# Optimization experiments

Hardware: AMD Instinct MI355X
Metric: run time of the kernel (lower is better)

## Reference

```python
import jax, jax.numpy as jnp
import numpy as np

N, M, C, IN, OUT = 65536, 512, 512, 256, 256
EPS = 1e-8


def setup_inputs() -> dict:
    key = jax.random.key(0)
    ks = jax.random.split(key, 12)
    d = {}
    d["x"] = jax.random.normal(ks[0], (1, IN), jnp.float32)
    d["memory"] = jax.random.normal(ks[1], (1, N, M), jnp.float32) * 0.05
    d["prev_read"] = jax.random.normal(ks[2], (1, M), jnp.float32) * 0.05
    d["h"] = jnp.ones((1, C), jnp.float32)
    d["c"] = jnp.ones((1, C), jnp.float32)
    d["read_state"] = jnp.zeros((1, N), jnp.float32)
    d["write_state"] = jnp.zeros((1, N), jnp.float32)
    d["W_ih"] = jax.random.normal(ks[3], (4 * C, IN + M), jnp.float32) * 0.02
    d["b_ih"] = jax.random.normal(ks[4], (4 * C,), jnp.float32) * 0.01
    d["W_hh"] = jax.random.normal(ks[5], (4 * C, C), jnp.float32) * 0.02
    d["b_hh"] = jax.random.normal(ks[6], (4 * C,), jnp.float32) * 0.01
    d["W_read"] = jax.random.normal(ks[7], (M + 6, C), jnp.float32) * 0.02
    d["b_read"] = jnp.zeros((M + 6,), jnp.float32)
    d["W_write"] = jax.random.normal(ks[8], (3 * M + 6, C), jnp.float32) * 0.02
    d["b_write"] = jnp.zeros((3 * M + 6,), jnp.float32)
    d["W_out"] = jax.random.normal(ks[9], (OUT, C + M), jnp.float32) * 0.02
    d["b_out"] = jnp.zeros((OUT,), jnp.float32)
    return d


def _address(head_out, w_prev, memory):
    # head_out: [B, M+6(+...)]; returns sharpened addressing weights [B, N]
    key_v = head_out[:, :M]
    beta = jax.nn.softplus(head_out[:, M:M + 1])          # [B,1]
    g = jax.nn.sigmoid(head_out[:, M + 1:M + 2])          # [B,1]
    shift = jax.nn.softmax(head_out[:, M + 2:M + 5], axis=1)  # [B,3]
    gamma = 1.0 + jax.nn.softplus(head_out[:, M + 5:M + 6])   # [B,1]
    # content addressing: cosine similarity over memory rows
    a = memory + EPS                                      # [B,N,M]
    b = key_v[:, None, :] + EPS                           # [B,1,M]
    dot = jnp.sum(a * b, axis=-1)                         # [B,N]
    na = jnp.maximum(jnp.sqrt(jnp.sum(a * a, axis=-1)), EPS)
    nb = jnp.maximum(jnp.sqrt(jnp.sum(b * b, axis=-1)), EPS)
    cos = dot / (na * nb)
    w_context = jax.nn.softmax(beta * cos, axis=1)        # [B,N]
    # NOTE: original code swaps args -> g gates the PREVIOUS weights
    w_interp = g * w_prev + (1.0 - g) * w_context
    # circular shift via 3-tap correlation (conv1d with circular pad)
    w_pad = jnp.concatenate([w_interp[:, -1:], w_interp, w_interp[:, :1]], axis=1)
    w_shift = (w_pad[:, :-2] * shift[:, 0:1]
               + w_pad[:, 1:-1] * shift[:, 1:2]
               + w_pad[:, 2:] * shift[:, 2:3])
    power = w_shift ** gamma
    return power / (jnp.sum(power, axis=1, keepdims=True) + EPS)


def reference(x, memory, prev_read, h, c, read_state, write_state,
              W_ih, b_ih, W_hh, b_hh, W_read, b_read, W_write, b_write,
              W_out, b_out):
    # LSTMCell controller (torch gate order: i, f, g, o)
    inp = jnp.concatenate([x, prev_read], axis=1)                   # [B, IN+M]
    gates = inp @ W_ih.T + b_ih + h @ W_hh.T + b_hh                 # [B, 4C]
    i_g, f_g, g_g, o_g = jnp.split(gates, 4, axis=1)
    c_new = jax.nn.sigmoid(f_g) * c + jax.nn.sigmoid(i_g) * jnp.tanh(g_g)
    h_new = jax.nn.sigmoid(o_g) * jnp.tanh(c_new)

    # read head
    r_out = h_new @ W_read.T + b_read
    w_r = _address(r_out, read_state, memory)                       # [B,N]
    # faithful to torch.matmul([B,N],[B,N,M]).sum(1): sums weights over batch
    read = jnp.einsum('n,bnm->bm', jnp.sum(w_r, axis=0), memory)    # [B,M]

    # write head
    w_out_head = h_new @ W_write.T + b_write
    w_w = _address(w_out_head, write_state, memory)                 # [B,N]
    erase = jax.nn.sigmoid(w_out_head[:, M + 6:2 * M + 6])          # [B,M]
    add = w_out_head[:, 2 * M + 6:3 * M + 6]                        # [B,M]
    memory_new = memory * (1.0 - w_w[:, :, None] * erase[:, None, :]) \
                 + w_w[:, :, None] * add[:, None, :]                # [B,N,M]

    out = jax.nn.sigmoid(jnp.concatenate([h_new, read], axis=1) @ W_out.T + b_out)
    del memory_new  # state update; torch forward returns only the output
    return out
```

## Files before the change

### kernel.cpp

```cpp
#include <hip/hip_runtime.h>
#include <math.h>

#define EPS 1e-8f
#define NN 65536
#define MAGIC 1.0f

#define WS_GATES 0
#define WS_HNEW  2048
#define WS_ROUT  2560
#define WS_PMAX  3104
#define WS_PEXP  5152
#define WS_S     7200
#define WS_PART  72992
#define WS_FLAGG 204064
#define WS_FLAGP 204192
#define WS_PART2 204448
#define WS_FLAG2 220832
#define WS_BF    262144
#define WS_PARTB 17039360
#define WS_PSUMB 18087936

typedef float f32x2 __attribute__((ext_vector_type(2)));

__device__ __forceinline__ float wave_sum(float v) {
    for (int o = 32; o > 0; o >>= 1) v += __shfl_xor(v, o);
    return v;
}
__device__ __forceinline__ float sigm(float x) { return 1.f / (1.f + expf(-x)); }
__device__ __forceinline__ float softplusf_(float x) {
    return x > 20.f ? x : log1pf(expf(x));
}
__device__ __forceinline__ float dot4(float4 a, float4 b) {
    return a.x * b.x + a.y * b.y + a.z * b.z + a.w * b.w;
}
__device__ __forceinline__ float4 ld4(const float* p) { return *(const float4*)p; }

__device__ __forceinline__ float ald(const float* p) {
    return __hip_atomic_load(p, __ATOMIC_RELAXED, __HIP_MEMORY_SCOPE_AGENT);
}
__device__ __forceinline__ float ald_acq(const float* p) {
    return __hip_atomic_load(p, __ATOMIC_ACQUIRE, __HIP_MEMORY_SCOPE_AGENT);
}
__device__ __forceinline__ void ast(float* p, float v) {
    __hip_atomic_store(p, v, __ATOMIC_RELAXED, __HIP_MEMORY_SCOPE_AGENT);
}
__device__ __forceinline__ void ast_rel(float* p, float v) {
    __hip_atomic_store(p, v, __ATOMIC_RELEASE, __HIP_MEMORY_SCOPE_AGENT);
}

__device__ __forceinline__ unsigned pk8(float4 v) {
    int u = __builtin_amdgcn_cvt_pk_fp8_f32(v.x, v.y, 0, false);
    u = __builtin_amdgcn_cvt_pk_fp8_f32(v.z, v.w, u, true);
    return (unsigned)u;
}

__global__ __launch_bounds__(256) void k_front(const float* __restrict__ x,
                                               const float* __restrict__ pr,
                                               const float* __restrict__ h,
                                               const float* __restrict__ c,
                                               const float* __restrict__ W_ih,
                                               const float* __restrict__ b_ih,
                                               const float* __restrict__ W_hh,
                                               const float* __restrict__ b_hh,
                                               const float* __restrict__ W_read,
                                               const float* __restrict__ b_read,
                                               float* __restrict__ ws) {
    const int b = blockIdx.x, t = threadIdx.x;
    const int lane = t & 63, wv = t >> 6;
    __shared__ float sh[512];

    if (b < 128) {
        #pragma unroll
        for (int i = 0; i < 4; ++i) {
            const int row = b * 16 + wv * 4 + i;
            const float* wi = W_ih + (size_t)row * 768;
            const float* wh = W_hh + (size_t)row * 512;
            float acc = dot4(ld4(wi + lane * 4), ld4(x + lane * 4))
                      + dot4(ld4(wi + 256 + lane * 4), ld4(pr + lane * 4))
                      + dot4(ld4(wi + 512 + lane * 4), ld4(pr + 256 + lane * 4))
                      + dot4(ld4(wh + lane * 4), ld4(h + lane * 4))
                      + dot4(ld4(wh + 256 + lane * 4), ld4(h + 256 + lane * 4));
            acc = wave_sum(acc);
            if (lane == 0) ast(ws + WS_GATES + row, acc + b_ih[row] + b_hh[row]);
        }
        __syncthreads();
        if (t == 0) ast_rel(ws + WS_FLAGG + b, MAGIC);
    }

    if (wv == 0) {
        int cap = 0;
        for (;;) {
            float v0 = ald_acq(ws + WS_FLAGG + lane);
            float v1 = ald_acq(ws + WS_FLAGG + 64 + lane);
            if (__all(v0 == MAGIC && v1 == MAGIC)) break;
            __builtin_amdgcn_s_sleep(1);
            if (++cap > (1 << 20)) break;
        }
    }
    __syncthreads();

    for (int j = t; j < 512; j += 256) {
        float ig = ald(ws + WS_GATES + j);
        float fg = ald(ws + WS_GATES + 512 + j);
        float gg = ald(ws + WS_GATES + 1024 + j);
        float og = ald(ws + WS_GATES + 1536 + j);
        float cn = sigm(fg) * c[j] + sigm(ig) * tanhf(gg);
        float hn = sigm(og) * tanhf(cn);
        sh[j] = hn;
        if (b == 0) ws[WS_HNEW + j] = hn;
    }
    __syncthreads();
    const int o = b * 4 + wv;
    if (o < 518) {
        const float* wr = W_read + (size_t)o * 512;
        float acc = dot4(ld4(wr + lane * 4), ld4(sh + lane * 4))
                  + dot4(ld4(wr + 256 + lane * 4), ld4(sh + 256 + lane * 4));
        acc = wave_sum(acc);
        if (lane == 0) ws[WS_ROUT + o] = acc + b_read[o];
    }
}

__global__ __launch_bounds__(256) void k_cos(const float* __restrict__ mem,
                                             float* __restrict__ ws) {
    const int t = threadIdx.x, lane = t & 63, wv = t >> 6;
    const int gw = blockIdx.x * 4 + wv;
    const float* key = ws + WS_ROUT;
    unsigned char* wsb = (unsigned char*)(ws + WS_BF);
    float4 ka = ld4(key + lane * 4);
    float4 kb = ld4(key + 256 + lane * 4);
    ka.x += EPS; ka.y += EPS; ka.z += EPS; ka.w += EPS;
    kb.x += EPS; kb.y += EPS; kb.z += EPS; kb.w += EPS;
    const float nb = fmaxf(__builtin_amdgcn_sqrtf(
                        wave_sum(dot4(ka, ka) + dot4(kb, kb))), EPS);
    const float beta = softplusf_(key[512]);
    float* sp = ws + WS_S;

    float4 va[4], vb[4], xa[4], xb[4];
    #pragma unroll
    for (int i = 0; i < 4; ++i) {
        const size_t n = (size_t)gw + i * 8192;
        va[i] = ld4(mem + n * 512 + lane * 4);
        vb[i] = ld4(mem + n * 512 + 256 + lane * 4);
    }
    #pragma unroll
    for (int i = 0; i < 4; ++i) {
        const size_t n = (size_t)gw + (4 + i) * 8192;
        xa[i] = ld4(mem + n * 512 + lane * 4);
        xb[i] = ld4(mem + n * 512 + 256 + lane * 4);
    }

    float m = -1e30f, e = 0.f;
    #pragma unroll
    for (int grp = 0; grp < 2; ++grp) {
        float d[4], q[4];
        #pragma unroll
        for (int i = 0; i < 4; ++i) {
            const size_t n = (size_t)gw + (grp * 4 + i) * 8192;
            *(unsigned*)(wsb + n * 512 + lane * 4) = pk8(va[i]);
            *(unsigned*)(wsb + n * 512 + 256 + lane * 4) = pk8(vb[i]);
            float4 wa = va[i], wb = vb[i];
            wa.x += EPS; wa.y += EPS; wa.z += EPS; wa.w += EPS;
            wb.x += EPS; wb.y += EPS; wb.z += EPS; wb.w += EPS;
            d[i] = dot4(wa, ka) + dot4(wb, kb);
            q[i] = dot4(wa, wa) + dot4(wb, wb);
        }
        if (grp == 0) {
            #pragma unroll
            for (int i = 0; i < 4; ++i) { va[i] = xa[i]; vb[i] = xb[i]; }
        }
        #pragma unroll
        for (int o = 32; o > 0; o >>= 1) {
            #pragma unroll
            for (int i = 0; i < 4; ++i) {
                d[i] += __shfl_xor(d[i], o);
                q[i] += __shfl_xor(q[i], o);
            }
        }
        float sv[4];
        #pragma unroll
        for (int i = 0; i < 4; ++i) {
            float na = fmaxf(__builtin_amdgcn_sqrtf(q[i]), EPS);
            sv[i] = beta * d[i] * __builtin_amdgcn_rcpf(na * nb);
        }
        float mysv = sv[0];
        if (lane == 1) mysv = sv[1];
        if (lane == 2) mysv = sv[2];
        if (lane == 3) mysv = sv[3];
        if (lane < 4) sp[gw + (grp * 4 + lane) * 8192] = mysv;
        float gm = fmaxf(fmaxf(sv[0], sv[1]), fmaxf(sv[2], sv[3]));
        float nm = fmaxf(m, gm);
        e = e * __expf(m - nm) + __expf(sv[0] - nm) + __expf(sv[1] - nm)
          + __expf(sv[2] - nm) + __expf(sv[3] - nm);
        m = nm;
    }

    __shared__ float sm[4], se[4];
    if (lane == 0) { sm[wv] = m; se[wv] = e; }
    __syncthreads();
    if (t == 0) {
        float M = fmaxf(fmaxf(sm[0], sm[1]), fmaxf(sm[2], sm[3]));
        float E = se[0] * __expf(sm[0] - M) + se[1] * __expf(sm[1] - M) +
                  se[2] * __expf(sm[2] - M) + se[3] * __expf(sm[3] - M);
        ws[WS_PMAX + blockIdx.x] = M;
        ws[WS_PEXP + blockIdx.x] = E;
    }
}

__global__ __launch_bounds__(256) void k_read(const float* __restrict__ rs,
                                              float* __restrict__ ws) {
    const int bb = blockIdx.x, t = threadIdx.x;
    const int lane = t & 63, wv = t >> 6;
    __shared__ float s_m[4], s_e[4];
    __shared__ float wi_l[34];
    __shared__ float pl[32];
    __shared__ float sacc[3][512];

    float m = -1e30f, e = 0.f;
    #pragma unroll
    for (int i = 0; i < 8; ++i) {
        float bm = ws[WS_PMAX + t + 256 * i], be = ws[WS_PEXP + t + 256 * i];
        float nm = fmaxf(m, bm);
        e = e * __expf(m - nm) + be * __expf(bm - nm);
        m = nm;
    }
    for (int o = 32; o > 0; o >>= 1) {
        float om = __shfl_xor(m, o), oe = __shfl_xor(e, o);
        float nm = fmaxf(m, om);
        e = e * __expf(m - nm) + oe * __expf(om - nm);
        m = nm;
    }
    if (lane == 0) { s_m[wv] = m; s_e[wv] = e; }
    __syncthreads();
    const float mx = fmaxf(fmaxf(s_m[0], s_m[1]), fmaxf(s_m[2], s_m[3]));
    const float Z = s_e[0] * __expf(s_m[0] - mx) + s_e[1] * __expf(s_m[1] - mx)
                  + s_e[2] * __expf(s_m[2] - mx) + s_e[3] * __expf(s_m[3] - mx);
    const float invZ = 1.f / Z;
    const float g = sigm(ws[WS_ROUT + 513]);
    float a3 = ws[WS_ROUT + 514], b3 = ws[WS_ROUT + 515], c3 = ws[WS_ROUT + 516];
    float mm = fmaxf(a3, fmaxf(b3, c3));
    float ea = __expf(a3 - mm), eb = __expf(b3 - mm), ec = __expf(c3 - mm);
    float ss = ea + eb + ec;
    const float s0 = ea / ss, s1 = eb / ss, s2 = ec / ss;
    const float gamma = 1.f + softplusf_(ws[WS_ROUT + 517]);

    const int start = bb * 32;
    if (t < 34) {
        int idx = (start - 1 + t) & (NN - 1);
        wi_l[t] = g * rs[idx] + (1.f - g) * __expf(ws[WS_S + idx] - mx) * invZ;
    }
    __syncthreads();
    float ps = 0.f;
    if (t < 32) {
        float wsh = wi_l[t] * s0 + wi_l[t + 1] * s1 + wi_l[t + 2] * s2;
        float pv = __powf(wsh, gamma);
        pl[t] = pv;
        ps = pv;
    }
    ps = wave_sum(ps);
    if (t == 0) ws[WS_PSUMB + bb] = ps;
    __syncthreads();

    const unsigned char* slab =
        (const unsigned char*)(ws + WS_BF) + (size_t)(start + wv * 8) * 512;
    float a0 = 0.f, a1 = 0.f, a2 = 0.f, a3f = 0.f,
          a4 = 0.f, a5 = 0.f, a6 = 0.f, a7 = 0.f;
    #pragma unroll
    for (int r = 0; r < 8; ++r) {
        float w = pl[wv * 8 + r];
        uint2 q = *(const uint2*)(slab + (size_t)r * 512 + lane * 8);
        f32x2 f0 = __builtin_amdgcn_cvt_pk_f32_fp8(q.x, false);
        f32x2 f1 = __builtin_amdgcn_cvt_pk_f32_fp8(q.x, true);
        f32x2 f2 = __builtin_amdgcn_cvt_pk_f32_fp8(q.y, false);
        f32x2 f3 = __builtin_amdgcn_cvt_pk_f32_fp8(q.y, true);
        a0 += w * f0.x;  a1 += w * f0.y;
        a2 += w * f1.x;  a3f += w * f1.y;
        a4 += w * f2.x;  a5 += w * f2.y;
        a6 += w * f3.x;  a7 += w * f3.y;
    }
    if (wv) {
        float* sw = sacc[wv - 1];
        sw[0 * 64 + lane] = a0; sw[1 * 64 + lane] = a1;
        sw[2 * 64 + lane] = a2; sw[3 * 64 + lane] = a3f;
        sw[4 * 64 + lane] = a4; sw[5 * 64 + lane] = a5;
        sw[6 * 64 + lane] = a6; sw[7 * 64 + lane] = a7;
    }
    __syncthreads();
    if (!wv) {
        #pragma unroll
        for (int i = 0; i < 3; ++i) {
            const float* sw = sacc[i];
            a0 += sw[0 * 64 + lane]; a1 += sw[1 * 64 + lane];
            a2 += sw[2 * 64 + lane]; a3f += sw[3 * 64 + lane];
            a4 += sw[4 * 64 + lane]; a5 += sw[5 * 64 + lane];
            a6 += sw[6 * 64 + lane]; a7 += sw[7 * 64 + lane];
        }
        float* pp = ws + WS_PARTB + (size_t)bb * 512 + lane * 8;
        *(float4*)pp = make_float4(a0, a1, a2, a3f);
        *(float4*)(pp + 4) = make_float4(a4, a5, a6, a7);
    }
}

__global__ __launch_bounds__(512) void k_out(const float* __restrict__ W_out,
                                             const float* __restrict__ b_out,
                                             float* __restrict__ ws,
                                             float* __restrict__ out) {
    const int b = blockIdx.x, t = threadIdx.x;
    const int lane = t & 63, wv = t >> 6;
    __shared__ float rd[512];
    __shared__ float s_z[8];

    {
        float s = 0.f;
        #pragma unroll
        for (int r = 0; r < 8; ++r)
            s += ws[WS_PARTB + (size_t)(8 * b + r) * 512 + t];
        ws[WS_PART + (size_t)b * 512 + t] = s;
    }
    __syncthreads();
    if (t == 0) ast_rel(ws + WS_FLAGP + b, MAGIC);
    if (b >= 32) return;

    if (wv == 0) {
        int cap = 0;
        for (;;) {
            float v0 = ald_acq(ws + WS_FLAGP + lane);
            float v1 = ald_acq(ws + WS_FLAGP + 64 + lane);
            float v2 = ald_acq(ws + WS_FLAGP + 128 + lane);
            float v3 = ald_acq(ws + WS_FLAGP + 192 + lane);
            if (__all(v0 == MAGIC && v1 == MAGIC && v2 == MAGIC && v3 == MAGIC))
                break;
            __builtin_amdgcn_s_sleep(1);
            if (++cap > (1 << 20)) break;
        }
    }
    __syncthreads();
    {
        float s = 0.f;
        #pragma unroll
        for (int r = 0; r < 8; ++r)
            s += ws[WS_PART + (size_t)(8 * b + r) * 512 + t];
        ws[WS_PART2 + (size_t)b * 512 + t] = s;
    }
    __syncthreads();
    if (t == 0) ast_rel(ws + WS_FLAG2 + b, MAGIC);
    if (wv == 0) {
        int cap = 0;
        for (;;) {
            float v = ald_acq(ws + WS_FLAG2 + (lane & 31));
            if (__all(v == MAGIC)) break;
            __builtin_amdgcn_s_sleep(1);
            if (++cap > (1 << 20)) break;
        }
    }
    __syncthreads();
    float z = 0.f;
    #pragma unroll
    for (int i = 0; i < 4; ++i) z += ws[WS_PSUMB + t + 512 * i];
    z = wave_sum(z);
    if (lane == 0) s_z[wv] = z;
    __syncthreads();
    float Zp = 0.f;
    for (int i = 0; i < 8; ++i) Zp += s_z[i];
    const float invZp = 1.f / (Zp + EPS);
    {
        float s = 0.f;
        #pragma unroll
        for (int r = 0; r < 32; ++r)
            s += ws[WS_PART2 + (size_t)r * 512 + t];
        rd[t] = s * invZp;
    }
    __syncthreads();
    const int o = b * 8 + wv;
    const float* wo = W_out + (size_t)o * 1024;
    float a = dot4(ld4(wo + lane * 4), ld4(ws + WS_HNEW + lane * 4))
            + dot4(ld4(wo + 256 + lane * 4), ld4(ws + WS_HNEW + 256 + lane * 4))
            + dot4(ld4(wo + 512 + lane * 4), ld4(rd + lane * 4))
            + dot4(ld4(wo + 768 + lane * 4), ld4(rd + 256 + lane * 4));
    a = wave_sum(a);
    if (lane == 0) out[o] = sigm(a + b_out[o]);
}

extern "C" void kernel_launch(void* const* d_in, const int* in_sizes, int n_in,
                              void* d_out, int out_size, void* d_ws, size_t ws_size,
                              hipStream_t stream) {
    const float* x          = (const float*)d_in[0];
    const float* memory     = (const float*)d_in[1];
    const float* prev_read  = (const float*)d_in[2];
    const float* h          = (const float*)d_in[3];
    const float* c          = (const float*)d_in[4];
    const float* read_state = (const float*)d_in[5];
    const float* W_ih   = (const float*)d_in[7];
    const float* b_ih   = (const float*)d_in[8];
    const float* W_hh   = (const float*)d_in[9];
    const float* b_hh   = (const float*)d_in[10];
    const float* W_read = (const float*)d_in[11];
    const float* b_read = (const float*)d_in[12];
    const float* W_out  = (const float*)d_in[15];
    const float* b_out  = (const float*)d_in[16];
    float* ws  = (float*)d_ws;
    float* out = (float*)d_out;

    k_front<<<130, 256, 0, stream>>>(x, prev_read, h, c, W_ih, b_ih, W_hh, b_hh,
                                     W_read, b_read, ws);
    k_cos<<<2048, 256, 0, stream>>>(memory, ws);
    k_read<<<2048, 256, 0, stream>>>(read_state, ws);
    k_out<<<256, 512, 0, stream>>>(W_out, b_out, ws, out);
}
```

Measured before the change: 66.48 us.

## Fuse four kernels into two using flag-based inter-block synchronization

Merges the LSTM/read-projection front kernel into the cosine-similarity kernel, and the read-accumulation kernel into the output kernel. Workgroups spin on global release/acquire flags in place of kernel boundaries. This removes two launch gaps and their tail drain. In exchange, 2048 blocks now all wait on flags set by the first 130 (and later the first 2048). That relies on enough blocks being co-resident or scheduled in order, and costs polling traffic plus idle waiting blocks.

```diff
diff --git a/kernel.cpp b/kernel.cpp
--- a/kernel.cpp
+++ b/kernel.cpp
@@ -16,9 +16,11 @@
 #define WS_FLAGP 204192
 #define WS_PART2 204448
 #define WS_FLAG2 220832
+#define WS_FLAGR 220864
 #define WS_BF    262144
 #define WS_PARTB 17039360
 #define WS_PSUMB 18087936
+#define WS_FLAGB 18089984
 
 typedef float f32x2 __attribute__((ext_vector_type(2)));
 
@@ -54,17 +56,18 @@
     return (unsigned)u;
 }
 
-__global__ __launch_bounds__(256) void k_front(const float* __restrict__ x,
-                                               const float* __restrict__ pr,
-                                               const float* __restrict__ h,
-                                               const float* __restrict__ c,
-                                               const float* __restrict__ W_ih,
-                                               const float* __restrict__ b_ih,
-                                               const float* __restrict__ W_hh,
-                                               const float* __restrict__ b_hh,
-                                               const float* __restrict__ W_read,
-                                               const float* __restrict__ b_read,
-                                               float* __restrict__ ws) {
+__global__ __launch_bounds__(256) void k_fc(const float* __restrict__ x,
+                                            const float* __restrict__ pr,
+                                            const float* __restrict__ h,
+                                            const float* __restrict__ c,
+                                            const float* __restrict__ W_ih,
+                                            const float* __restrict__ b_ih,
+                                            const float* __restrict__ W_hh,
+                                            const float* __restrict__ b_hh,
+                                            const float* __restrict__ W_read,
+                                            const float* __restrict__ b_read,
+                                            const float* __restrict__ mem,
+                                            float* __restrict__ ws) {
     const int b = blockIdx.x, t = threadIdx.x;
     const int lane = t & 63, wv = t >> 6;
     __shared__ float sh[512];
@@ -87,43 +90,55 @@
         if (t == 0) ast_rel(ws + WS_FLAGG + b, MAGIC);
     }
 
+    if (b < 130) {
+        if (wv == 0) {
+            int cap = 0;
+            for (;;) {
+                float v0 = ald_acq(ws + WS_FLAGG + lane);
+                float v1 = ald_acq(ws + WS_FLAGG + 64 + lane);
+                if (__all(v0 == MAGIC && v1 == MAGIC)) break;
+                __builtin_amdgcn_s_sleep(1);
+                if (++cap > (1 << 20)) break;
+            }
+        }
+        __syncthreads();
+        for (int j = t; j < 512; j += 256) {
+            float ig = ald(ws + WS_GATES + j);
+            float fg = ald(ws + WS_GATES + 512 + j);
+            float gg = ald(ws + WS_GATES + 1024 + j);
+            float og = ald(ws + WS_GATES + 1536 + j);
+            float cn = sigm(fg) * c[j] + sigm(ig) * tanhf(gg);
+            float hn = sigm(og) * tanhf(cn);
+            sh[j] = hn;
+            if (b == 0) ws[WS_HNEW + j] = hn;
+        }
+        __syncthreads();
+        const int o = b * 4 + wv;
+        if (o < 518) {
+            const float* wr = W_read + (size_t)o * 512;
+            float acc = dot4(ld4(wr + lane * 4), ld4(sh + lane * 4))
+                      + dot4(ld4(wr + 256 + lane * 4), ld4(sh + 256 + lane * 4));
+            acc = wave_sum(acc);
+            if (lane == 0) ws[WS_ROUT + o] = acc + b_read[o];
+        }
+        __syncthreads();
+        if (t == 0) ast_rel(ws + WS_FLAGR + b, MAGIC);
+    }
+
     if (wv == 0) {
         int cap = 0;
         for (;;) {
-            float v0 = ald_acq(ws + WS_FLAGG + lane);
-            float v1 = ald_acq(ws + WS_FLAGG + 64 + lane);
-            if (__all(v0 == MAGIC && v1 == MAGIC)) break;
+            float v0 = ald_acq(ws + WS_FLAGR + lane);
+            float v1 = ald_acq(ws + WS_FLAGR + 64 + lane);
+            float v2 = ald_acq(ws + WS_FLAGR + 128 + (lane & 1));
+            if (__all(v0 == MAGIC && v1 == MAGIC && v2 == MAGIC)) break;
             __builtin_amdgcn_s_sleep(1);
             if (++cap > (1 << 20)) break;
         }
     }
     __syncthreads();
 
-    for (int j = t; j < 512; j += 256) {
-        float ig = ald(ws + WS_GATES + j);
-        float fg = ald(ws + WS_GATES + 512 + j);
-        float gg = ald(ws + WS_GATES + 1024 + j);
-        float og = ald(ws + WS_GATES + 1536 + j);
-        float cn = sigm(fg) * c[j] + sigm(ig) * tanhf(gg);
-        float hn = sigm(og) * tanhf(cn);
-        sh[j] = hn;
-        if (b == 0) ws[WS_HNEW + j] = hn;
-    }
-    __syncthreads();
-    const int o = b * 4 + wv;
-    if (o < 518) {
-        const float* wr = W_read + (size_t)o * 512;
-        float acc = dot4(ld4(wr + lane * 4), ld4(sh + lane * 4))
-                  + dot4(ld4(wr + 256 + lane * 4), ld4(sh + 256 + lane * 4));
-        acc = wave_sum(acc);
-        if (lane == 0) ws[WS_ROUT + o] = acc + b_read[o];
-    }
-}
-
-__global__ __launch_bounds__(256) void k_cos(const float* __restrict__ mem,
-                                             float* __restrict__ ws) {
-    const int t = threadIdx.x, lane = t & 63, wv = t >> 6;
-    const int gw = blockIdx.x * 4 + wv;
+    const int gw = b * 4 + wv;
     const float* key = ws + WS_ROUT;
     unsigned char* wsb = (unsigned char*)(ws + WS_BF);
     float4 ka = ld4(key + lane * 4);
@@ -201,19 +216,24 @@
         float M = fmaxf(fmaxf(sm[0], sm[1]), fmaxf(sm[2], sm[3]));
         float E = se[0] * __expf(sm[0] - M) + se[1] * __expf(sm[1] - M) +
                   se[2] * __expf(sm[2] - M) + se[3] * __expf(sm[3] - M);
-        ws[WS_PMAX + blockIdx.x] = M;
-        ws[WS_PEXP + blockIdx.x] = E;
-    }
-}
-
-__global__ __launch_bounds__(256) void k_read(const float* __restrict__ rs,
-                                              float* __restrict__ ws) {
+        ws[WS_PMAX + b] = M;
+        ws[WS_PEXP + b] = E;
+    }
+}
+
+__global__ __launch_bounds__(256) void k_ro(const float* __restrict__ rs,
+                                            const float* __restrict__ W_out,
+                                            const float* __restrict__ b_out,
+                                            float* __restrict__ ws,
+                                            float* __restrict__ out) {
     const int bb = blockIdx.x, t = threadIdx.x;
     const int lane = t & 63, wv = t >> 6;
     __shared__ float s_m[4], s_e[4];
     __shared__ float wi_l[34];
     __shared__ float pl[32];
     __shared__ float sacc[3][512];
+    __shared__ float rd[512];
+    __shared__ float s_z[4];
 
     float m = -1e30f, e = 0.f;
     #pragma unroll
@@ -260,66 +280,76 @@
     if (t == 0) ws[WS_PSUMB + bb] = ps;
     __syncthreads();
 
-    const unsigned char* slab =
-        (const unsigned char*)(ws + WS_BF) + (size_t)(start + wv * 8) * 512;
-    float a0 = 0.f, a1 = 0.f, a2 = 0.f, a3f = 0.f,
-          a4 = 0.f, a5 = 0.f, a6 = 0.f, a7 = 0.f;
-    #pragma unroll
-    for (int r = 0; r < 8; ++r) {
-        float w = pl[wv * 8 + r];
-        uint2 q = *(const uint2*)(slab + (size_t)r * 512 + lane * 8);
-        f32x2 f0 = __builtin_amdgcn_cvt_pk_f32_fp8(q.x, false);
-        f32x2 f1 = __builtin_amdgcn_cvt_pk_f32_fp8(q.x, true);
-        f32x2 f2 = __builtin_amdgcn_cvt_pk_f32_fp8(q.y, false);
-        f32x2 f3 = __builtin_amdgcn_cvt_pk_f32_fp8(q.y, true);
-        a0 += w * f0.x;  a1 += w * f0.y;
-        a2 += w * f1.x;  a3f += w * f1.y;
-        a4 += w * f2.x;  a5 += w * f2.y;
-        a6 += w * f3.x;  a7 += w * f3.y;
-    }
-    if (wv) {
-        float* sw = sacc[wv - 1];
-        sw[0 * 64 + lane] = a0; sw[1 * 64 + lane] = a1;
-        sw[2 * 64 + lane] = a2; sw[3 * 64 + lane] = a3f;
-        sw[4 * 64 + lane] = a4; sw[5 * 64 + lane] = a5;
-        sw[6 * 64 + lane] = a6; sw[7 * 64 + lane] = a7;
-    }
-    __syncthreads();
-    if (!wv) {
-        #pragma unroll
-        for (int i = 0; i < 3; ++i) {
-            const float* sw = sacc[i];
-            a0 += sw[0 * 64 + lane]; a1 += sw[1 * 64 + lane];
-            a2 += sw[2 * 64 + lane]; a3f += sw[3 * 64 + lane];
-            a4 += sw[4 * 64 + lane]; a5 += sw[5 * 64 + lane];
-            a6 += sw[6 * 64 + lane]; a7 += sw[7 * 64 + lane];
-        }
-        float* pp = ws + WS_PARTB + (size_t)bb * 512 + lane * 8;
-        *(float4*)pp = make_float4(a0, a1, a2, a3f);
-        *(float4*)(pp + 4) = make_float4(a4, a5, a6, a7);
-    }
-}
-
-__global__ __launch_bounds__(512) void k_out(const float* __restrict__ W_out,
-                                             const float* __restrict__ b_out,
-                                             float* __restrict__ ws,
-                                             float* __restrict__ out) {
-    const int b = blockIdx.x, t = threadIdx.x;
-    const int lane = t & 63, wv = t >> 6;
-    __shared__ float rd[512];
-    __shared__ float s_z[8];
-
     {
+        const unsigned char* slab =
+            (const unsigned char*)(ws + WS_BF) + (size_t)(start + wv * 8) * 512;
+        float a0 = 0.f, a1 = 0.f, a2 = 0.f, a3f = 0.f,
+              a4 = 0.f, a5 = 0.f, a6 = 0.f, a7 = 0.f;
+        #pragma unroll
+        for (int r = 0; r < 8; ++r) {
+            float w = pl[wv * 8 + r];
+            uint2 q = *(const uint2*)(slab + (size_t)r * 512 + lane * 8);
+            f32x2 f0 = __builtin_amdgcn_cvt_pk_f32_fp8(q.x, false);
+            f32x2 f1 = __builtin_amdgcn_cvt_pk_f32_fp8(q.x, true);
+            f32x2 f2 = __builtin_amdgcn_cvt_pk_f32_fp8(q.y, false);
+            f32x2 f3 = __builtin_amdgcn_cvt_pk_f32_fp8(q.y, true);
+            a0 += w * f0.x;  a1 += w * f0.y;
+            a2 += w * f1.x;  a3f += w * f1.y;
+            a4 += w * f2.x;  a5 += w * f2.y;
+            a6 += w * f3.x;  a7 += w * f3.y;
+        }
+        if (wv) {
+            float* sw = sacc[wv - 1];
+            sw[0 * 64 + lane] = a0; sw[1 * 64 + lane] = a1;
+            sw[2 * 64 + lane] = a2; sw[3 * 64 + lane] = a3f;
+            sw[4 * 64 + lane] = a4; sw[5 * 64 + lane] = a5;
+            sw[6 * 64 + lane] = a6; sw[7 * 64 + lane] = a7;
+        }
+        __syncthreads();
+        if (!wv) {
+            #pragma unroll
+            for (int i = 0; i < 3; ++i) {
+                const float* sw = sacc[i];
+                a0 += sw[0 * 64 + lane]; a1 += sw[1 * 64 + lane];
+                a2 += sw[2 * 64 + lane]; a3f += sw[3 * 64 + lane];
+                a4 += sw[4 * 64 + lane]; a5 += sw[5 * 64 + lane];
+                a6 += sw[6 * 64 + lane]; a7 += sw[7 * 64 + lane];
+            }
+            float* pp = ws + WS_PARTB + (size_t)bb * 512 + lane * 8;
+            *(float4*)pp = make_float4(a0, a1, a2, a3f);
+            *(float4*)(pp + 4) = make_float4(a4, a5, a6, a7);
+        }
+    }
+    __syncthreads();
+    if (t == 0) ast_rel(ws + WS_FLAGB + bb, MAGIC);
+
+    if (bb >= 256) return;
+    if (wv == 0) {
+        int cap = 0;
+        for (;;) {
+            bool ok = true;
+            #pragma unroll
+            for (int k = 0; k < 32; ++k)
+                ok &= (ald_acq(ws + WS_FLAGB + k * 64 + lane) == MAGIC);
+            if (__all(ok)) break;
+            __builtin_amdgcn_s_sleep(1);
+            if (++cap > (1 << 20)) break;
+        }
+    }
+    __syncthreads();
+    #pragma unroll
+    for (int cc = 0; cc < 2; ++cc) {
+        const int col = t + cc * 256;
         float s = 0.f;
         #pragma unroll
         for (int r = 0; r < 8; ++r)
-            s += ws[WS_PARTB + (size_t)(8 * b + r) * 512 + t];
-        ws[WS_PART + (size_t)b * 512 + t] = s;
-    }
-    __syncthreads();
-    if (t == 0) ast_rel(ws + WS_FLAGP + b, MAGIC);
-    if (b >= 32) return;
-
+            s += ws[WS_PARTB + (size_t)(8 * bb + r) * 512 + col];
+        ws[WS_PART + (size_t)bb * 512 + col] = s;
+    }
+    __syncthreads();
+    if (t == 0) ast_rel(ws + WS_FLAGP + bb, MAGIC);
+
+    if (bb >= 32) return;
     if (wv == 0) {
         int cap = 0;
         for (;;) {
@@ -334,15 +364,17 @@
         }
     }
     __syncthreads();
-    {
+    #pragma unroll
+    for (int cc = 0; cc < 2; ++cc) {
+        const int col = t + cc * 256;
         float s = 0.f;
         #pragma unroll
         for (int r = 0; r < 8; ++r)
-            s += ws[WS_PART + (size_t)(8 * b + r) * 512 + t];
-        ws[WS_PART2 + (size_t)b * 512 + t] = s;
-    }
-    __syncthreads();
-    if (t == 0) ast_rel(ws + WS_FLAG2 + b, MAGIC);
+            s += ws[WS_PART + (size_t)(8 * bb + r) * 512 + col];
+        ws[WS_PART2 + (size_t)bb * 512 + col] = s;
+    }
+    __syncthreads();
+    if (t == 0) ast_rel(ws + WS_FLAG2 + bb, MAGIC);
     if (wv == 0) {
         int cap = 0;
         for (;;) {
@@ -355,29 +387,33 @@
     __syncthreads();
     float z = 0.f;
     #pragma unroll
-    for (int i = 0; i < 4; ++i) z += ws[WS_PSUMB + t + 512 * i];
+    for (int i = 0; i < 8; ++i) z += ws[WS_PSUMB + t + 256 * i];
     z = wave_sum(z);
     if (lane == 0) s_z[wv] = z;
     __syncthreads();
-    float Zp = 0.f;
-    for (int i = 0; i < 8; ++i) Zp += s_z[i];
+    const float Zp = s_z[0] + s_z[1] + s_z[2] + s_z[3];
     const float invZp = 1.f / (Zp + EPS);
-    {
+    #pragma unroll
+    for (int cc = 0; cc < 2; ++cc) {
+        const int col = t + cc * 256;
         float s = 0.f;
         #pragma unroll
         for (int r = 0; r < 32; ++r)
-            s += ws[WS_PART2 + (size_t)r * 512 + t];
-        rd[t] = s * invZp;
-    }
-    __syncthreads();
-    const int o = b * 8 + wv;
-    const float* wo = W_out + (size_t)o * 1024;
-    float a = dot4(ld4(wo + lane * 4), ld4(ws + WS_HNEW + lane * 4))
-            + dot4(ld4(wo + 256 + lane * 4), ld4(ws + WS_HNEW + 256 + lane * 4))
-            + dot4(ld4(wo + 512 + lane * 4), ld4(rd + lane * 4))
-            + dot4(ld4(wo + 768 + lane * 4), ld4(rd + 256 + lane * 4));
-    a = wave_sum(a);
-    if (lane == 0) out[o] = sigm(a + b_out[o]);
+            s += ws[WS_PART2 + (size_t)r * 512 + col];
+        rd[col] = s * invZp;
+    }
+    __syncthreads();
+    #pragma unroll
+    for (int j = 0; j < 2; ++j) {
+        const int o = bb * 8 + wv * 2 + j;
+        const float* wo = W_out + (size_t)o * 1024;
+        float a = dot4(ld4(wo + lane * 4), ld4(ws + WS_HNEW + lane * 4))
+                + dot4(ld4(wo + 256 + lane * 4), ld4(ws + WS_HNEW + 256 + lane * 4))
+                + dot4(ld4(wo + 512 + lane * 4), ld4(rd + lane * 4))
+                + dot4(ld4(wo + 768 + lane * 4), ld4(rd + 256 + lane * 4));
+        a = wave_sum(a);
+        if (lane == 0) out[o] = sigm(a + b_out[o]);
+    }
 }
 
 extern "C" void kernel_launch(void* const* d_in, const int* in_sizes, int n_in,
@@ -400,9 +436,7 @@
     float* ws  = (float*)d_ws;
     float* out = (float*)d_out;
 
-    k_front<<<130, 256, 0, stream>>>(x, prev_read, h, c, W_ih, b_ih, W_hh, b_hh,
-                                     W_read, b_read, ws);
-    k_cos<<<2048, 256, 0, stream>>>(memory, ws);
-    k_read<<<2048, 256, 0, stream>>>(read_state, ws);
-    k_out<<<256, 512, 0, stream>>>(W_out, b_out, ws, out);
-}
+    k_fc<<<2048, 256, 0, stream>>>(x, prev_read, h, c, W_ih, b_ih, W_hh, b_hh,
+                                   W_read, b_read, memory, ws);
+    k_ro<<<2048, 256, 0, stream>>>(read_state, W_out, b_out, ws, out);
+}
```

After: 211.3 us. 3.18x slower.
